# Optimization experiments

Hardware: AMD Instinct MI355X
Metric: run time of the kernel (lower is better)

The kernel has to match this reference:

```python
import jax, jax.numpy as jnp
import numpy as np
from jax import lax

B_, H_, W_ = 2, 32, 32
D_MODEL, D_STATE, D_CONV, DT_RANK, K = 192, 16, 3, 12, 4
D_INNER = 2 * D_MODEL


def setup_inputs() -> dict:
    key = jax.random.key(0)
    ks = jax.random.split(key, 10)
    x = jax.random.normal(ks[0], (B_, H_, W_, D_MODEL), jnp.float32)
    x_cross = jax.random.normal(ks[1], (B_, H_, W_, D_MODEL), jnp.float32)
    in_proj_w = jax.random.normal(ks[2], (2 * D_INNER, D_MODEL), jnp.float32) * 0.02
    in_proj_cross_w = jax.random.normal(ks[3], (D_INNER, D_MODEL), jnp.float32) * 0.02
    conv_w = jax.random.normal(ks[4], (D_INNER, 1, D_CONV, D_CONV), jnp.float32) * 0.1  # depthwise
    conv_b = jnp.zeros((D_INNER,), jnp.float32)
    x_proj_weight = jax.random.normal(ks[5], (K, DT_RANK + 2 * D_STATE, D_INNER), jnp.float32) * 0.02
    dt_std = DT_RANK ** -0.5
    dt_projs_weight = jax.random.uniform(ks[6], (K, D_INNER, DT_RANK), jnp.float32, -dt_std, dt_std)
    # inverse-softplus init of dt bias, as in CSS2D.dt_init
    dt = jnp.exp(jax.random.uniform(ks[7], (K, D_INNER), jnp.float32)
                 * (np.log(0.1) - np.log(0.001)) + np.log(0.001))
    dt = jnp.clip(dt, 1e-4, None)
    dt_projs_bias = dt + jnp.log(-jnp.expm1(-dt))
    A_logs = jnp.log(jnp.tile(jnp.arange(1, D_STATE + 1, dtype=jnp.float32)[None, :], (K * D_INNER, 1)))
    Ds = jnp.ones((K * D_INNER,), jnp.float32)
    out_norm_g = jnp.ones((D_INNER,), jnp.float32)
    out_norm_b = jnp.zeros((D_INNER,), jnp.float32)
    out_proj_w = jax.random.normal(ks[8], (D_MODEL, D_INNER), jnp.float32) * 0.02
    return dict(x=x, x_cross=x_cross, in_proj_w=in_proj_w, in_proj_cross_w=in_proj_cross_w,
                conv_w=conv_w, conv_b=conv_b, x_proj_weight=x_proj_weight,
                dt_projs_weight=dt_projs_weight, dt_projs_bias=dt_projs_bias,
                A_logs=A_logs, Ds=Ds, out_norm_g=out_norm_g, out_norm_b=out_norm_b,
                out_proj_w=out_proj_w)


def _css2d_forward(x, x_cross, in_proj_w, in_proj_cross_w, conv_w, conv_b,
                   x_proj_weight, dt_projs_weight, dt_projs_bias, A_logs, Ds,
                   out_norm_g, out_norm_b, out_proj_w):
    B, H, W, _ = x.shape
    L = H * W
    Din, N, R = D_INNER, D_STATE, DT_RANK

    # in projections
    xz = x @ in_proj_w.T                       # [B,H,W,2*Din]
    xp, z = jnp.split(xz, 2, axis=-1)
    xc = x_cross @ in_proj_cross_w.T           # [B,H,W,Din]

    # depthwise conv + SiLU on main branch (NCHW)
    xh = jnp.transpose(xp, (0, 3, 1, 2))
    pad = (D_CONV - 1) // 2
    xh = lax.conv_general_dilated(xh, conv_w, (1, 1), [(pad, pad), (pad, pad)],
                                  dimension_numbers=('NCHW', 'OIHW', 'NCHW'),
                                  feature_group_count=Din)
    xh = jax.nn.silu(xh + conv_b[None, :, None, None])
    xc = jnp.transpose(xc, (0, 3, 1, 2))       # [B,Din,H,W]

    def cross_scan(t):  # [B,Din,H,W] -> [B,4,Din,L]
        a = t.reshape(B, Din, L)
        b = jnp.transpose(t, (0, 1, 3, 2)).reshape(B, Din, L)
        s = jnp.stack([a, b], axis=1)
        return jnp.concatenate([s, jnp.flip(s, axis=-1)], axis=1)

    xs = cross_scan(xh)
    xsc = cross_scan(xc)

    # dt/B/C projections from the cross stream
    x_dbl = jnp.einsum('bkdl,kcd->bkcl', xsc, x_proj_weight)
    dts, Bmat, Cmat = jnp.split(x_dbl, [R, R + N], axis=2)  # [B,K,R,L],[B,K,N,L],[B,K,N,L]
    dts = jnp.einsum('bkrl,kdr->bkdl', dts, dt_projs_weight)

    A = -jnp.exp(A_logs).reshape(K, Din, N)
    delta = jax.nn.softplus(dts + dt_projs_bias[None, :, :, None])  # [B,K,Din,L]

    # selective scan: h_{t} = exp(delta*A)*h_{t-1} + delta*B_t*u_t ; y_t = C_t . h_t
    dA = jnp.exp(jnp.einsum('bkdl,kdn->lbkdn', delta, A))   # [L,B,K,Din,N]
    dBu = jnp.einsum('bkdl,bknl->lbkdn', delta * xs, Bmat)  # [L,B,K,Din,N]
    Ct = jnp.transpose(Cmat, (3, 0, 1, 2))                  # [L,B,K,N]

    def step(h, inp):
        dA_t, dBu_t, c = inp
        h = dA_t * h + dBu_t
        return h, jnp.einsum('bkdn,bkn->bkd', h, c)

    h0 = jnp.zeros((B, K, Din, N), x.dtype)
    _, ys = lax.scan(step, h0, (dA, dBu, Ct))               # ys: [L,B,K,Din]
    out_y = jnp.transpose(ys, (1, 2, 3, 0)) + xs * Ds.reshape(1, K, Din, 1)  # [B,K,Din,L]

    # merge the 4 directions
    inv_y = jnp.flip(out_y[:, 2:4], axis=-1)
    wh = lambda t: jnp.transpose(t.reshape(B, Din, W, H), (0, 1, 3, 2)).reshape(B, Din, L)
    y = out_y[:, 0] + inv_y[:, 0] + wh(out_y[:, 1]) + wh(inv_y[:, 1])
    y = jnp.transpose(y, (0, 2, 1)).reshape(B, H, W, Din)

    # LayerNorm(out_norm)
    mu = jnp.mean(y, axis=-1, keepdims=True)
    var = jnp.mean((y - mu) ** 2, axis=-1, keepdims=True)
    y = (y - mu) * lax.rsqrt(var + 1e-5) * out_norm_g + out_norm_b

    y = y * jax.nn.silu(z)
    return y @ out_proj_w.T


def reference(x, x_cross, in_proj_w, in_proj_cross_w, conv_w, conv_b, x_proj_weight,
              dt_projs_weight, dt_projs_bias, A_logs, Ds, out_norm_g, out_norm_b, out_proj_w):
    return _css2d_forward(x, x_cross, in_proj_w, in_proj_cross_w, conv_w, conv_b,
                          x_proj_weight, dt_projs_weight, dt_projs_bias, A_logs, Ds,
                          out_norm_g, out_norm_b, out_proj_w)
```

## Files before the change

kernel.cpp:

```cpp
#include <hip/hip_runtime.h>
#include <hip/hip_bf16.h>
#include <math.h>

#define BB 2
#define HH 32
#define WW 32
#define LL 1024
#define DM 192
#define DI 384
#define NS 16
#define RR 12
#define KK 4
#define CC 44
#define NC 64
#define LC 16
#define NCH 3072
#define GB 49152
#define XT 8

__device__ __forceinline__ int bfflag(const void* dsv){
  return ((const unsigned*)dsv)[0] != 0x3F800000u;
}
__device__ __forceinline__ float ldin(const void* p, int i, int bf) {
  if (bf) {
    unsigned v = ((const unsigned short*)p)[i];
    return __uint_as_float(v << 16);
  }
  return ((const float*)p)[i];
}
__device__ __forceinline__ float4 ldin4(const void* p, int i, int bf) {
  if (bf) {
    ushort4 u = ((const ushort4*)p)[i >> 2];
    float4 r;
    r.x = __uint_as_float((unsigned)u.x << 16);
    r.y = __uint_as_float((unsigned)u.y << 16);
    r.z = __uint_as_float((unsigned)u.z << 16);
    r.w = __uint_as_float((unsigned)u.w << 16);
    return r;
  }
  return ((const float4*)p)[i >> 2];
}
__device__ __forceinline__ float sigm(float x){ return 1.f/(1.f + __expf(-x)); }
__device__ __forceinline__ float softplusf(float x){ return (x > 20.f) ? x : log1pf(__expf(x)); }

__device__ __forceinline__ int permk(int k, int l){
  if (k == 0) return l;
  if (k == 2) return LL-1-l;
  int lr = (k == 3) ? (LL-1-l) : l;
  return (lr & 31)*WW + (lr >> 5);
}

__global__ __launch_bounds__(256) void k_inproj(const void* x, const void* xcr,
    const void* wi, const void* wc, const void* dsv,
    float* __restrict__ xp, float* __restrict__ z, float* __restrict__ xcd){
  const int bf = bfflag(dsv);
  __shared__ float As[64][65];
  __shared__ float Ws[64][65];
  const int mb = blockIdx.x & 31;
  const int nb = blockIdx.x >> 5;
  const int pos0 = mb*64;
  const int row0g = nb*64;
  const void* src  = (row0g < 768) ? x  : xcr;
  const void* wsrc = (row0g < 768) ? wi : wc;
  const int wrow0 = (row0g < 768) ? row0g : row0g - 768;
  const int t = threadIdx.x;
  const int tx = t & 15, ty = t >> 4;
  float acc[4][4];
  #pragma unroll
  for (int m=0;m<4;m++){
    #pragma unroll
    for (int n=0;n<4;n++) acc[m][n]=0.f;
  }
  for (int k0 = 0; k0 < DM; k0 += 64){
    for (int i = t*4; i < 4096; i += 1024){
      const int p = i >> 6, kk = i & 63;
      const float4 va = ldin4(src,  (pos0 +p)*DM + k0 + kk, bf);
      As[kk+0][p]=va.x; As[kk+1][p]=va.y; As[kk+2][p]=va.z; As[kk+3][p]=va.w;
      const float4 vw = ldin4(wsrc, (wrow0+p)*DM + k0 + kk, bf);
      Ws[kk+0][p]=vw.x; Ws[kk+1][p]=vw.y; Ws[kk+2][p]=vw.z; Ws[kk+3][p]=vw.w;
    }
    __syncthreads();
    #pragma unroll 8
    for (int kk = 0; kk < 64; kk++){
      const float4 a4 = *(const float4*)&As[kk][ty*4];
      const float4 w4 = *(const float4*)&Ws[kk][tx*4];
      acc[0][0]=fmaf(a4.x,w4.x,acc[0][0]); acc[0][1]=fmaf(a4.x,w4.y,acc[0][1]);
      acc[0][2]=fmaf(a4.x,w4.z,acc[0][2]); acc[0][3]=fmaf(a4.x,w4.w,acc[0][3]);
      acc[1][0]=fmaf(a4.y,w4.x,acc[1][0]); acc[1][1]=fmaf(a4.y,w4.y,acc[1][1]);
      acc[1][2]=fmaf(a4.y,w4.z,acc[1][2]); acc[1][3]=fmaf(a4.y,w4.w,acc[1][3]);
      acc[2][0]=fmaf(a4.z,w4.x,acc[2][0]); acc[2][1]=fmaf(a4.z,w4.y,acc[2][1]);
      acc[2][2]=fmaf(a4.z,w4.z,acc[2][2]); acc[2][3]=fmaf(a4.z,w4.w,acc[2][3]);
      acc[3][0]=fmaf(a4.w,w4.x,acc[3][0]); acc[3][1]=fmaf(a4.w,w4.y,acc[3][1]);
      acc[3][2]=fmaf(a4.w,w4.z,acc[3][2]); acc[3][3]=fmaf(a4.w,w4.w,acc[3][3]);
    }
    __syncthreads();
  }
  float* dst; int obase;
  if (row0g < 384)      { dst = xp;  obase = row0g; }
  else if (row0g < 768) { dst = z;   obase = row0g-384; }
  else                  { dst = xcd; obase = row0g-768; }
  #pragma unroll
  for (int m=0;m<4;m++){
    const int pos = pos0 + ty*4 + m;
    *(float4*)&dst[(size_t)pos*DI + obase + tx*4] =
        make_float4(acc[m][0], acc[m][1], acc[m][2], acc[m][3]);
  }
}

__global__ __launch_bounds__(256) void k_conv(const float* __restrict__ xp,
    const void* cw, const void* cb, const void* dsv, float* __restrict__ xh){
  const int bf = bfflag(dsv);
  const int idx = blockIdx.x*256 + threadIdx.x;
  const int d = idx % DI;
  const int l = (idx / DI) % LL;
  const int b = idx / (DI*LL);
  const int h = l >> 5, w = l & 31;
  float acc = ldin(cb, d, bf);
  #pragma unroll
  for (int kh=0; kh<3; kh++){
    const int hh = h + kh - 1;
    if (hh < 0 || hh >= HH) continue;
    #pragma unroll
    for (int kw=0; kw<3; kw++){
      const int ww2 = w + kw - 1;
      if (ww2 < 0 || ww2 >= WW) continue;
      acc = fmaf(xp[(b*LL + hh*WW + ww2)*DI + d], ldin(cw, d*9 + kh*3 + kw, bf), acc);
    }
  }
  xh[idx] = acc * sigm(acc);
}

__global__ __launch_bounds__(384) void k_xproj(const float* __restrict__ xc, const void* xpw,
    const void* dtw, const void* dtb, const void* dsv,
    float* __restrict__ delta, float* __restrict__ Bm, float* __restrict__ Cm){
  const int bf = bfflag(dsv);
  const int blk = blockIdx.x;
  const int b = blk >> 9;
  const int k = (blk >> 7) & 3;
  const int l0 = (blk & 127) * XT;
  const int t = threadIdx.x;
  __shared__ float xrow[XT][DI+4];
  __shared__ float dtsS[XT][RR];
  for (int idx = t; idx < XT*96; idx += 384){
    const int j = idx / 96, c = idx % 96;
    const int pl = permk(k, l0 + j);
    *(float4*)&xrow[j][c*4] = *(const float4*)&xc[(b*LL + pl)*DI + c*4];
  }
  __syncthreads();
  if (t < CC*XT){
    const int ch = t >> 3, j = t & 7;
    const int wbase = (k*CC + ch)*DI;
    float a0=0.f, a1=0.f, a2=0.f, a3=0.f;
    for (int c = 0; c < 96; c += 4){
      const float4 w0 = ldin4(xpw, wbase + (c+0)*4, bf);
      const float4 w1 = ldin4(xpw, wbase + (c+1)*4, bf);
      const float4 w2 = ldin4(xpw, wbase + (c+2)*4, bf);
      const float4 w3 = ldin4(xpw, wbase + (c+3)*4, bf);
      const float4 x0 = *(const float4*)&xrow[j][(c+0)*4];
      const float4 x1 = *(const float4*)&xrow[j][(c+1)*4];
      const float4 x2 = *(const float4*)&xrow[j][(c+2)*4];
      const float4 x3 = *(const float4*)&xrow[j][(c+3)*4];
      a0 = fmaf(w0.x,x0.x, fmaf(w0.y,x0.y, fmaf(w0.z,x0.z, fmaf(w0.w,x0.w, a0))));
      a1 = fmaf(w1.x,x1.x, fmaf(w1.y,x1.y, fmaf(w1.z,x1.z, fmaf(w1.w,x1.w, a1))));
      a2 = fmaf(w2.x,x2.x, fmaf(w2.y,x2.y, fmaf(w2.z,x2.z, fmaf(w2.w,x2.w, a2))));
      a3 = fmaf(w3.x,x3.x, fmaf(w3.y,x3.y, fmaf(w3.z,x3.z, fmaf(w3.w,x3.w, a3))));
    }
    const float acc = (a0+a1)+(a2+a3);
    if (ch < RR)           dtsS[j][ch] = acc;
    else if (ch < RR+NS)   Bm[((b*KK+k)*LL + l0+j)*NS + (ch-RR)]    = acc;
    else                   Cm[((b*KK+k)*LL + l0+j)*NS + (ch-RR-NS)] = acc;
  }
  __syncthreads();
  {
    const int d = t;
    float w[RR];
    #pragma unroll
    for (int q = 0; q < 3; q++){
      const float4 w4 = ldin4(dtw, (k*DI+d)*RR + q*4, bf);
      w[q*4+0]=w4.x; w[q*4+1]=w4.y; w[q*4+2]=w4.z; w[q*4+3]=w4.w;
    }
    const float bias = ldin(dtb, k*DI + d, bf);
    #pragma unroll
    for (int j = 0; j < XT; j++){
      float acc = bias;
      #pragma unroll
      for (int r = 0; r < RR; r++) acc = fmaf(w[r], dtsS[j][r], acc);
      xrow[j][d] = softplusf(acc);
    }
  }
  __syncthreads();
  for (int idx = t; idx < XT*96; idx += 384){
    const int j = idx / 96, c = idx % 96;
    *(float4*)&delta[((b*KK+k)*LL + l0+j)*DI + c*4] = *(const float4*)&xrow[j][c*4];
  }
}

__global__ __launch_bounds__(256) void k_scanA(const float* __restrict__ delta,
    const float* __restrict__ xh, const float* __restrict__ Bm,
    const void* alogs, const void* dsv,
    float* __restrict__ Acum, float* __restrict__ Hend){
  const int bf = bfflag(dsv);
  const int c = blockIdx.x / 12;
  const int chain = (blockIdx.x % 12)*256 + threadIdx.x;
  const int d = chain % DI;
  const int k = (chain / DI) & 3;
  const int b = chain / (DI*KK);
  float An[NS];
  #pragma unroll
  for (int q = 0; q < 4; q++){
    const float4 a4 = ldin4(alogs, (k*DI + d)*NS + q*4, bf);
    An[q*4+0] = -__expf(a4.x); An[q*4+1] = -__expf(a4.y);
    An[q*4+2] = -__expf(a4.z); An[q*4+3] = -__expf(a4.w);
  }
  float h[NS], Ac[NS];
  #pragma unroll
  for (int n = 0; n < NS; n++){ h[n] = 0.f; Ac[n] = 1.f; }
  const int lb = (b*KK+k)*LL;
  const int xbase = b*LL*DI + d;
  const int l0 = c*LC;
  #pragma unroll 4
  for (int l = l0; l < l0+LC; l++){
    const float dl = delta[(lb + l)*DI + d];
    const float u  = xh[xbase + permk(k,l)*DI];
    const float dlu = dl*u;
    const float4 B0 = *(const float4*)&Bm[(lb+l)*NS + 0];
    const float4 B1 = *(const float4*)&Bm[(lb+l)*NS + 4];
    const float4 B2 = *(const float4*)&Bm[(lb+l)*NS + 8];
    const float4 B3 = *(const float4*)&Bm[(lb+l)*NS + 12];
    const float Bv[NS] = {B0.x,B0.y,B0.z,B0.w, B1.x,B1.y,B1.z,B1.w,
                          B2.x,B2.y,B2.z,B2.w, B3.x,B3.y,B3.z,B3.w};
    #pragma unroll
    for (int n = 0; n < NS; n++){
      const float e = __expf(dl*An[n]);
      Ac[n] *= e;
      h[n] = fmaf(e, h[n], dlu*Bv[n]);
    }
  }
  const int obase = (c*NCH + chain)*NS;
  #pragma unroll
  for (int q = 0; q < 4; q++){
    *(float4*)&Acum[obase + q*4] = make_float4(Ac[q*4],Ac[q*4+1],Ac[q*4+2],Ac[q*4+3]);
    *(float4*)&Hend[obase + q*4] = make_float4(h[q*4],h[q*4+1],h[q*4+2],h[q*4+3]);
  }
}

__global__ __launch_bounds__(256) void k_scanB(const float* __restrict__ Acum,
    float* __restrict__ Hend){
  const int g = blockIdx.x*256 + threadIdx.x;
  float h = 0.f;
  #pragma unroll 8
  for (int c = 0; c < NC; c++){
    const float a = Acum[c*GB + g];
    const float e = Hend[c*GB + g];
    Hend[c*GB + g] = h;
    h = fmaf(a, h, e);
  }
}

__global__ __launch_bounds__(256) void k_scanC(const float* __restrict__ delta,
    const float* __restrict__ xh, const float* __restrict__ Bm,
    const float* __restrict__ Cm, const void* alogs, const void* dsv,
    const float* __restrict__ Hin, float* __restrict__ ybuf){
  const int bf = bfflag(dsv);
  const int c = blockIdx.x / 12;
  const int chain = (blockIdx.x % 12)*256 + threadIdx.x;
  const int d = chain % DI;
  const int k = (chain / DI) & 3;
  const int b = chain / (DI*KK);
  float An[NS];
  #pragma unroll
  for (int q = 0; q < 4; q++){
    const float4 a4 = ldin4(alogs, (k*DI + d)*NS + q*4, bf);
    An[q*4+0] = -__expf(a4.x); An[q*4+1] = -__expf(a4.y);
    An[q*4+2] = -__expf(a4.z); An[q*4+3] = -__expf(a4.w);
  }
  float h[NS];
  const int ibase = (c*NCH + chain)*NS;
  #pragma unroll
  for (int q = 0; q < 4; q++){
    const float4 h4 = *(const float4*)&Hin[ibase + q*4];
    h[q*4+0]=h4.x; h[q*4+1]=h4.y; h[q*4+2]=h4.z; h[q*4+3]=h4.w;
  }
  const int lb = (b*KK+k)*LL;
  const int xbase = b*LL*DI + d;
  const int l0 = c*LC;
  #pragma unroll 4
  for (int l = l0; l < l0+LC; l++){
    const float dl = delta[(lb + l)*DI + d];
    const float u  = xh[xbase + permk(k,l)*DI];
    const float dlu = dl*u;
    const float4 B0 = *(const float4*)&Bm[(lb+l)*NS + 0];
    const float4 B1 = *(const float4*)&Bm[(lb+l)*NS + 4];
    const float4 B2 = *(const float4*)&Bm[(lb+l)*NS + 8];
    const float4 B3 = *(const float4*)&Bm[(lb+l)*NS + 12];
    const float4 C0 = *(const float4*)&Cm[(lb+l)*NS + 0];
    const float4 C1 = *(const float4*)&Cm[(lb+l)*NS + 4];
    const float4 C2 = *(const float4*)&Cm[(lb+l)*NS + 8];
    const float4 C3 = *(const float4*)&Cm[(lb+l)*NS + 12];
    const float Bv[NS] = {B0.x,B0.y,B0.z,B0.w, B1.x,B1.y,B1.z,B1.w,
                          B2.x,B2.y,B2.z,B2.w, B3.x,B3.y,B3.z,B3.w};
    const float Cv[NS] = {C0.x,C0.y,C0.z,C0.w, C1.x,C1.y,C1.z,C1.w,
                          C2.x,C2.y,C2.z,C2.w, C3.x,C3.y,C3.z,C3.w};
    float y = 0.f;
    #pragma unroll
    for (int n = 0; n < NS; n++){
      const float e = __expf(dl*An[n]);
      h[n] = fmaf(e, h[n], dlu*Bv[n]);
      y = fmaf(h[n], Cv[n], y);
    }
    ybuf[(lb + l)*DI + d] = y;
  }
}

__global__ __launch_bounds__(256) void k_merge(const float* __restrict__ scanY,
    const float* __restrict__ xh, const float* __restrict__ z,
    const void* dsP, const void* gP, const void* bP, const void* woP,
    void* out){
  const int bf = bfflag(dsP);
  const int blk = blockIdx.x;
  const int t = threadIdx.x;
  const int wv = t >> 6, lane = t & 63;
  __shared__ float ygs[8][DI];
  #pragma unroll
  for (int rep = 0; rep < 2; rep++){
    const int j = wv*2 + rep;
    const int pos = blk*8 + j;
    const int b = pos >> 10, l = pos & 1023;
    const int lt = (l & 31)*32 + (l >> 5);
    float yv[6];
    float s = 0.f, s2 = 0.f;
    #pragma unroll
    for (int i = 0; i < 6; i++){
      const int d = i*64 + lane;
      float y = scanY[((b*KK+0)*LL + l        )*DI + d]
              + scanY[((b*KK+2)*LL + (LL-1-l ))*DI + d]
              + scanY[((b*KK+1)*LL + lt       )*DI + d]
              + scanY[((b*KK+3)*LL + (LL-1-lt))*DI + d];
      const float dsum = ldin(dsP, d, bf) + ldin(dsP, DI+d, bf)
                       + ldin(dsP, 2*DI+d, bf) + ldin(dsP, 3*DI+d, bf);
      y = fmaf(xh[(b*LL+l)*DI + d], dsum, y);
      yv[i] = y;
      s += y; s2 = fmaf(y, y, s2);
    }
    #pragma unroll
    for (int m = 1; m < 64; m <<= 1){
      s  += __shfl_xor(s,  m);
      s2 += __shfl_xor(s2, m);
    }
    const float mu = s * (1.f/DI);
    const float var = fmaxf(s2 * (1.f/DI) - mu*mu, 0.f);
    const float rs = rsqrtf(var + 1e-5f);
    #pragma unroll
    for (int i = 0; i < 6; i++){
      const int d = i*64 + lane;
      const float yn = (yv[i]-mu)*rs*ldin(gP, d, bf) + ldin(bP, d, bf);
      const float zg = z[(b*LL+l)*DI + d];
      ygs[j][d] = yn * zg * sigm(zg);
    }
  }
  __syncthreads();
  if (t < DM){
    const int o = t;
    float acc[8];
    #pragma unroll
    for (int j=0;j<8;j++) acc[j] = 0.f;
    for (int c = 0; c < 96; c++){
      const float4 w4 = ldin4(woP, o*DI + c*4, bf);
      #pragma unroll
      for (int j=0;j<8;j++){
        const float4 y4 = *(const float4*)&ygs[j][c*4];
        acc[j] = fmaf(w4.x, y4.x, acc[j]);
        acc[j] = fmaf(w4.y, y4.y, acc[j]);
        acc[j] = fmaf(w4.z, y4.z, acc[j]);
        acc[j] = fmaf(w4.w, y4.w, acc[j]);
      }
    }
    #pragma unroll
    for (int j=0;j<8;j++){
      const int pos = blk*8 + j;
      if (bf) ((__hip_bfloat16*)out)[pos*DM + o] = __float2bfloat16(acc[j]);
      else    ((float*)out)[pos*DM + o] = acc[j];
    }
  }
}

extern "C" void kernel_launch(void* const* d_in, const int* in_sizes, int n_in,
                              void* d_out, int out_size, void* d_ws, size_t ws_size,
                              hipStream_t stream){
  const void* x    = d_in[0];
  const void* xcr  = d_in[1];
  const void* wi   = d_in[2];
  const void* wc   = d_in[3];
  const void* cw   = d_in[4];
  const void* cb   = d_in[5];
  const void* xpw  = d_in[6];
  const void* dtw  = d_in[7];
  const void* dtb  = d_in[8];
  const void* alog = d_in[9];
  const void* dsv  = d_in[10];
  const void* gno  = d_in[11];
  const void* bno  = d_in[12];
  const void* wo   = d_in[13];

  float* ws = (float*)d_ws;
  float* xp    = ws + 16;
  float* z     = xp    + (size_t)BB*LL*DI;
  float* xc    = z     + (size_t)BB*LL*DI;
  float* xh    = xc    + (size_t)BB*LL*DI;
  float* delta = xh    + (size_t)BB*LL*DI;
  float* Bm    = delta + (size_t)BB*KK*LL*DI;
  float* Cm    = Bm    + (size_t)BB*KK*LL*NS;
  float* Acum  = Cm    + (size_t)BB*KK*LL*NS;
  float* Hend  = Acum  + (size_t)GB*NC;
  float* ybuf  = Hend  + (size_t)GB*NC;

  k_inproj<<<18*32, 256, 0, stream>>>(x, xcr, wi, wc, dsv, xp, z, xc);
  k_conv  <<<BB*LL*DI/256, 256, 0, stream>>>(xp, cw, cb, dsv, xh);
  k_xproj <<<BB*KK*(LL/XT), 384, 0, stream>>>(xc, xpw, dtw, dtb, dsv, delta, Bm, Cm);
  k_scanA <<<NCH*NC/256, 256, 0, stream>>>(delta, xh, Bm, alog, dsv, Acum, Hend);
  k_scanB <<<GB/256, 256, 0, stream>>>(Acum, Hend);
  k_scanC <<<NCH*NC/256, 256, 0, stream>>>(delta, xh, Bm, Cm, alog, dsv, Hend, ybuf);
  k_merge <<<BB*LL/8, 256, 0, stream>>>(ybuf, xh, z, dsv, gno, bno, wo, d_out);
}
```

Before: 231.6 us.

## Fuse x-projection with chunked scan phase A; shrink merge tile to four rows

The x-projection kernel now processes one 16-step chunk per block and directly runs the chunk-local scan (phase A) using delta and B held in shared memory. This removes a separate kernel launch and the global re-read of delta and B. The merge kernel now handles 4 positions per block instead of 8, doubling the block count for more parallelism at the cost of more weight reloads. The fused kernel has fewer blocks (512) and does serial per-thread scan work after the projection, so occupancy and overlap may suffer.

```diff
diff --git a/kernel.cpp b/kernel.cpp
--- a/kernel.cpp
+++ b/kernel.cpp
@@ -16,7 +16,6 @@
 #define LC 16
 #define NCH 3072
 #define GB 49152
-#define XT 8
 
 __device__ __forceinline__ int bfflag(const void* dsv){
   return ((const unsigned*)dsv)[0] != 0x3F800000u;
@@ -130,45 +129,50 @@
   xh[idx] = acc * sigm(acc);
 }
 
-__global__ __launch_bounds__(384) void k_xproj(const float* __restrict__ xc, const void* xpw,
-    const void* dtw, const void* dtb, const void* dsv,
-    float* __restrict__ delta, float* __restrict__ Bm, float* __restrict__ Cm){
+__global__ __launch_bounds__(384) void k_xscanA(const float* __restrict__ xc,
+    const float* __restrict__ xh, const void* xpw, const void* dtw,
+    const void* dtb, const void* alogs, const void* dsv,
+    float* __restrict__ delta, float* __restrict__ Bm, float* __restrict__ Cm,
+    float* __restrict__ Acum, float* __restrict__ Hend){
   const int bf = bfflag(dsv);
   const int blk = blockIdx.x;
-  const int b = blk >> 9;
-  const int k = (blk >> 7) & 3;
-  const int l0 = (blk & 127) * XT;
+  const int b = blk >> 8;
+  const int k = (blk >> 6) & 3;
+  const int c = blk & 63;
+  const int l0 = c * LC;
   const int t = threadIdx.x;
-  __shared__ float xrow[XT][DI+4];
-  __shared__ float dtsS[XT][RR];
-  for (int idx = t; idx < XT*96; idx += 384){
-    const int j = idx / 96, c = idx % 96;
+  __shared__ float xrow[LC][DI+4];
+  __shared__ float dtsS[LC][RR];
+  __shared__ float Bs[LC][NS];
+  for (int idx = t; idx < LC*96; idx += 384){
+    const int j = idx / 96, cc = idx % 96;
     const int pl = permk(k, l0 + j);
-    *(float4*)&xrow[j][c*4] = *(const float4*)&xc[(b*LL + pl)*DI + c*4];
+    *(float4*)&xrow[j][cc*4] = *(const float4*)&xc[(b*LL + pl)*DI + cc*4];
   }
   __syncthreads();
-  if (t < CC*XT){
-    const int ch = t >> 3, j = t & 7;
+  for (int idx = t; idx < CC*LC; idx += 384){
+    const int ch = idx >> 4, j = idx & 15;
     const int wbase = (k*CC + ch)*DI;
     float a0=0.f, a1=0.f, a2=0.f, a3=0.f;
-    for (int c = 0; c < 96; c += 4){
-      const float4 w0 = ldin4(xpw, wbase + (c+0)*4, bf);
-      const float4 w1 = ldin4(xpw, wbase + (c+1)*4, bf);
-      const float4 w2 = ldin4(xpw, wbase + (c+2)*4, bf);
-      const float4 w3 = ldin4(xpw, wbase + (c+3)*4, bf);
-      const float4 x0 = *(const float4*)&xrow[j][(c+0)*4];
-      const float4 x1 = *(const float4*)&xrow[j][(c+1)*4];
-      const float4 x2 = *(const float4*)&xrow[j][(c+2)*4];
-      const float4 x3 = *(const float4*)&xrow[j][(c+3)*4];
+    for (int cc = 0; cc < 96; cc += 4){
+      const float4 w0 = ldin4(xpw, wbase + (cc+0)*4, bf);
+      const float4 w1 = ldin4(xpw, wbase + (cc+1)*4, bf);
+      const float4 w2 = ldin4(xpw, wbase + (cc+2)*4, bf);
+      const float4 w3 = ldin4(xpw, wbase + (cc+3)*4, bf);
+      const float4 x0 = *(const float4*)&xrow[j][(cc+0)*4];
+      const float4 x1 = *(const float4*)&xrow[j][(cc+1)*4];
+      const float4 x2 = *(const float4*)&xrow[j][(cc+2)*4];
+      const float4 x3 = *(const float4*)&xrow[j][(cc+3)*4];
       a0 = fmaf(w0.x,x0.x, fmaf(w0.y,x0.y, fmaf(w0.z,x0.z, fmaf(w0.w,x0.w, a0))));
       a1 = fmaf(w1.x,x1.x, fmaf(w1.y,x1.y, fmaf(w1.z,x1.z, fmaf(w1.w,x1.w, a1))));
       a2 = fmaf(w2.x,x2.x, fmaf(w2.y,x2.y, fmaf(w2.z,x2.z, fmaf(w2.w,x2.w, a2))));
       a3 = fmaf(w3.x,x3.x, fmaf(w3.y,x3.y, fmaf(w3.z,x3.z, fmaf(w3.w,x3.w, a3))));
     }
     const float acc = (a0+a1)+(a2+a3);
-    if (ch < RR)           dtsS[j][ch] = acc;
-    else if (ch < RR+NS)   Bm[((b*KK+k)*LL + l0+j)*NS + (ch-RR)]    = acc;
-    else                   Cm[((b*KK+k)*LL + l0+j)*NS + (ch-RR-NS)] = acc;
+    if (ch < RR)          dtsS[j][ch] = acc;
+    else if (ch < RR+NS){ Bs[j][ch-RR] = acc;
+                          Bm[((b*KK+k)*LL + l0+j)*NS + (ch-RR)]    = acc; }
+    else                  Cm[((b*KK+k)*LL + l0+j)*NS + (ch-RR-NS)] = acc;
   }
   __syncthreads();
   {
@@ -181,7 +185,7 @@
     }
     const float bias = ldin(dtb, k*DI + d, bf);
     #pragma unroll
-    for (int j = 0; j < XT; j++){
+    for (int j = 0; j < LC; j++){
       float acc = bias;
       #pragma unroll
       for (int r = 0; r < RR; r++) acc = fmaf(w[r], dtsS[j][r], acc);
@@ -189,58 +193,43 @@
     }
   }
   __syncthreads();
-  for (int idx = t; idx < XT*96; idx += 384){
-    const int j = idx / 96, c = idx % 96;
-    *(float4*)&delta[((b*KK+k)*LL + l0+j)*DI + c*4] = *(const float4*)&xrow[j][c*4];
-  }
-}
-
-__global__ __launch_bounds__(256) void k_scanA(const float* __restrict__ delta,
-    const float* __restrict__ xh, const float* __restrict__ Bm,
-    const void* alogs, const void* dsv,
-    float* __restrict__ Acum, float* __restrict__ Hend){
-  const int bf = bfflag(dsv);
-  const int c = blockIdx.x / 12;
-  const int chain = (blockIdx.x % 12)*256 + threadIdx.x;
-  const int d = chain % DI;
-  const int k = (chain / DI) & 3;
-  const int b = chain / (DI*KK);
-  float An[NS];
-  #pragma unroll
-  for (int q = 0; q < 4; q++){
-    const float4 a4 = ldin4(alogs, (k*DI + d)*NS + q*4, bf);
-    An[q*4+0] = -__expf(a4.x); An[q*4+1] = -__expf(a4.y);
-    An[q*4+2] = -__expf(a4.z); An[q*4+3] = -__expf(a4.w);
-  }
-  float h[NS], Ac[NS];
-  #pragma unroll
-  for (int n = 0; n < NS; n++){ h[n] = 0.f; Ac[n] = 1.f; }
-  const int lb = (b*KK+k)*LL;
-  const int xbase = b*LL*DI + d;
-  const int l0 = c*LC;
-  #pragma unroll 4
-  for (int l = l0; l < l0+LC; l++){
-    const float dl = delta[(lb + l)*DI + d];
-    const float u  = xh[xbase + permk(k,l)*DI];
-    const float dlu = dl*u;
-    const float4 B0 = *(const float4*)&Bm[(lb+l)*NS + 0];
-    const float4 B1 = *(const float4*)&Bm[(lb+l)*NS + 4];
-    const float4 B2 = *(const float4*)&Bm[(lb+l)*NS + 8];
-    const float4 B3 = *(const float4*)&Bm[(lb+l)*NS + 12];
-    const float Bv[NS] = {B0.x,B0.y,B0.z,B0.w, B1.x,B1.y,B1.z,B1.w,
-                          B2.x,B2.y,B2.z,B2.w, B3.x,B3.y,B3.z,B3.w};
-    #pragma unroll
-    for (int n = 0; n < NS; n++){
-      const float e = __expf(dl*An[n]);
-      Ac[n] *= e;
-      h[n] = fmaf(e, h[n], dlu*Bv[n]);
-    }
-  }
-  const int obase = (c*NCH + chain)*NS;
-  #pragma unroll
-  for (int q = 0; q < 4; q++){
-    *(float4*)&Acum[obase + q*4] = make_float4(Ac[q*4],Ac[q*4+1],Ac[q*4+2],Ac[q*4+3]);
-    *(float4*)&Hend[obase + q*4] = make_float4(h[q*4],h[q*4+1],h[q*4+2],h[q*4+3]);
+  for (int idx = t; idx < LC*96; idx += 384){
+    const int j = idx / 96, cc = idx % 96;
+    *(float4*)&delta[((b*KK+k)*LL + l0+j)*DI + cc*4] = *(const float4*)&xrow[j][cc*4];
+  }
+  {
+    const int d = t;
+    float An[NS];
+    #pragma unroll
+    for (int q = 0; q < 4; q++){
+      const float4 a4 = ldin4(alogs, (k*DI + d)*NS + q*4, bf);
+      An[q*4+0] = -__expf(a4.x); An[q*4+1] = -__expf(a4.y);
+      An[q*4+2] = -__expf(a4.z); An[q*4+3] = -__expf(a4.w);
+    }
+    float h[NS], Ac[NS];
+    #pragma unroll
+    for (int n = 0; n < NS; n++){ h[n] = 0.f; Ac[n] = 1.f; }
+    const int xbase = b*LL*DI + d;
+    #pragma unroll 4
+    for (int j = 0; j < LC; j++){
+      const int l = l0 + j;
+      const float dl = xrow[j][d];
+      const float u  = xh[xbase + permk(k,l)*DI];
+      const float dlu = dl*u;
+      #pragma unroll
+      for (int n = 0; n < NS; n++){
+        const float e = __expf(dl*An[n]);
+        Ac[n] *= e;
+        h[n] = fmaf(e, h[n], dlu*Bs[j][n]);
+      }
+    }
+    const int chain = (b*KK + k)*DI + d;
+    const int obase = (c*NCH + chain)*NS;
+    #pragma unroll
+    for (int q = 0; q < 4; q++){
+      *(float4*)&Acum[obase + q*4] = make_float4(Ac[q*4],Ac[q*4+1],Ac[q*4+2],Ac[q*4+3]);
+      *(float4*)&Hend[obase + q*4] = make_float4(h[q*4],h[q*4+1],h[q*4+2],h[q*4+3]);
+    }
   }
 }
 
@@ -320,11 +309,10 @@
   const int blk = blockIdx.x;
   const int t = threadIdx.x;
   const int wv = t >> 6, lane = t & 63;
-  __shared__ float ygs[8][DI];
-  #pragma unroll
-  for (int rep = 0; rep < 2; rep++){
-    const int j = wv*2 + rep;
-    const int pos = blk*8 + j;
+  __shared__ float ygs[4][DI];
+  {
+    const int j = wv;
+    const int pos = blk*4 + j;
     const int b = pos >> 10, l = pos & 1023;
     const int lt = (l & 31)*32 + (l >> 5);
     float yv[6];
@@ -361,14 +349,14 @@
   __syncthreads();
   if (t < DM){
     const int o = t;
-    float acc[8];
-    #pragma unroll
-    for (int j=0;j<8;j++) acc[j] = 0.f;
-    for (int c = 0; c < 96; c++){
-      const float4 w4 = ldin4(woP, o*DI + c*4, bf);
+    float acc[4];
+    #pragma unroll
+    for (int j=0;j<4;j++) acc[j] = 0.f;
+    for (int cc = 0; cc < 96; cc++){
+      const float4 w4 = ldin4(woP, o*DI + cc*4, bf);
       #pragma unroll
-      for (int j=0;j<8;j++){
-        const float4 y4 = *(const float4*)&ygs[j][c*4];
+      for (int j=0;j<4;j++){
+        const float4 y4 = *(const float4*)&ygs[j][cc*4];
         acc[j] = fmaf(w4.x, y4.x, acc[j]);
         acc[j] = fmaf(w4.y, y4.y, acc[j]);
         acc[j] = fmaf(w4.z, y4.z, acc[j]);
@@ -376,8 +364,8 @@
       }
     }
     #pragma unroll
-    for (int j=0;j<8;j++){
-      const int pos = blk*8 + j;
+    for (int j=0;j<4;j++){
+      const int pos = blk*4 + j;
       if (bf) ((__hip_bfloat16*)out)[pos*DM + o] = __float2bfloat16(acc[j]);
       else    ((float*)out)[pos*DM + o] = acc[j];
     }
@@ -416,9 +404,9 @@
 
   k_inproj<<<18*32, 256, 0, stream>>>(x, xcr, wi, wc, dsv, xp, z, xc);
   k_conv  <<<BB*LL*DI/256, 256, 0, stream>>>(xp, cw, cb, dsv, xh);
-  k_xproj <<<BB*KK*(LL/XT), 384, 0, stream>>>(xc, xpw, dtw, dtb, dsv, delta, Bm, Cm);
-  k_scanA <<<NCH*NC/256, 256, 0, stream>>>(delta, xh, Bm, alog, dsv, Acum, Hend);
+  k_xscanA<<<BB*KK*NC, 384, 0, stream>>>(xc, xh, xpw, dtw, dtb, alog, dsv,
+                                         delta, Bm, Cm, Acum, Hend);
   k_scanB <<<GB/256, 256, 0, stream>>>(Acum, Hend);
   k_scanC <<<NCH*NC/256, 256, 0, stream>>>(delta, xh, Bm, Cm, alog, dsv, Hend, ybuf);
-  k_merge <<<BB*LL/8, 256, 0, stream>>>(ybuf, xh, z, dsv, gno, bno, wo, d_out);
-}
+  k_merge <<<BB*LL/4, 256, 0, stream>>>(ybuf, xh, z, dsv, gno, bno, wo, d_out);
+}
```

New measurement: 223.9 us. 1.03x faster.
